# Kernel optimization log

Hardware: AMD Instinct MI355X
Metric: run time of the kernel (lower is better)

The kernel has to match this reference:

```python
import jax, jax.numpy as jnp
import numpy as np

K = 5  # kernel_size hardcoded in Net
PAD = (K - 1) // 2


def _patches(x):
    # x: [B, C, H, W] -> [B, C, K*K, H, W] (zero-padded sliding windows, like nn.Unfold)
    B, C, H, W = x.shape
    xp = jnp.pad(x, ((0, 0), (0, 0), (PAD, PAD), (PAD, PAD)))
    return jnp.stack([xp[:, :, i:i + H, j:j + W]
                      for i in range(K) for j in range(K)], axis=2)


def setup_inputs() -> dict:
    key = jax.random.key(0)
    k1, k2, k3 = jax.random.split(key, 3)
    x = jax.random.uniform(k1, (16, 1, 512, 512), dtype=jnp.float32)
    noise_var = jax.random.uniform(k2, (1,), dtype=jnp.float32)
    noise_bias = jax.random.uniform(k3, (1,), dtype=jnp.float32)
    return {"x": x, "noise_var": noise_var, "noise_bias": noise_bias}


def reference(x, noise_var, noise_bias):
    p = _patches(x)                          # [B, C, 25, H, W]
    s_var = jnp.var(p, axis=2, ddof=1)       # torch.var is unbiased by default
    mid = jnp.median(p, axis=2)              # odd window -> exact middle element
    y = x - noise_var / (s_var + 1e-10) * (x - mid + noise_bias)
    return jax.nn.relu(y)
```

## Files before the change

### kernel.cpp

```cpp
#include <hip/hip_runtime.h>

#define PAD 2
#define PX 4
#define BDX 16
#define BDY 16
#define TSX (BDX * PX)
#define TSY BDY
#define LTW (TSX + 2 * PAD)
#define LTH (TSY + 2 * PAD)
#define NCHUNK (LTH * LTW / 4)

typedef float float4u __attribute__((vector_size(16), aligned(4)));
typedef float v4f __attribute__((ext_vector_type(4)));

__device__ __forceinline__ float min3f(float a, float b, float c) {
    float r; asm("v_min3_f32 %0, %1, %2, %3" : "=v"(r) : "v"(a), "v"(b), "v"(c)); return r;
}
__device__ __forceinline__ float max3f(float a, float b, float c) {
    float r; asm("v_max3_f32 %0, %1, %2, %3" : "=v"(r) : "v"(a), "v"(b), "v"(c)); return r;
}
__device__ __forceinline__ float med3f(float a, float b, float c) {
    float r; asm("v_med3_f32 %0, %1, %2, %3" : "=v"(r) : "v"(a), "v"(b), "v"(c)); return r;
}

#define CE(a, b) { float _lo = fminf(a, b), _hi = fmaxf(a, b); (a) = _lo; (b) = _hi; }

#define MED9(q0, q1, q2, q3, q4, q5, q6, q7, q8) \
    CE(q1, q2) CE(q4, q5) CE(q7, q8) \
    CE(q0, q1) CE(q3, q4) CE(q6, q7) \
    CE(q1, q2) CE(q4, q5) CE(q7, q8) \
    CE(q0, q3) CE(q5, q8) CE(q4, q7) \
    CE(q3, q6) CE(q1, q4) CE(q2, q5) \
    CE(q4, q7) CE(q4, q2) CE(q6, q4) \
    CE(q4, q2)

__global__ __launch_bounds__(256) void denoise_median5_kernel(
    const float* __restrict__ x,
    const float* __restrict__ noise_var_p,
    const float* __restrict__ noise_bias_p,
    float* __restrict__ out,
    int H, int W)
{
    __shared__ float tile[LTH][LTW];

    const float noise_var  = noise_var_p[0];
    const float noise_bias = noise_bias_p[0];

    const int b      = blockIdx.z;
    const int tile_y = blockIdx.y * TSY;
    const int tile_x = blockIdx.x * TSX;
    const int tx = threadIdx.x;
    const int ty = threadIdx.y;
    const int tid = ty * BDX + tx;

    const float* __restrict__ img = x + (size_t)b * H * W;

    const bool interior = (blockIdx.x > 0) && (blockIdx.x < gridDim.x - 1) &&
                          (blockIdx.y > 0) && (blockIdx.y < gridDim.y - 1);
    if (interior) {
        const float* gbase = img + (size_t)(tile_y - PAD) * W + (tile_x - PAD);
        {
            const int i = tid;
            const int row = i / 17;
            const int cc  = i - row * 17;
            float4u v = *(const float4u*)(gbase + (size_t)row * W + cc * 4);
            *(float4u*)&tile[row][cc * 4] = v;
        }
        if (tid < NCHUNK - 256) {
            const int i = tid + 256;
            const int row = i / 17;
            const int cc  = i - row * 17;
            float4u v = *(const float4u*)(gbase + (size_t)row * W + cc * 4);
            *(float4u*)&tile[row][cc * 4] = v;
        }
    } else {
        for (int i = tid; i < LTH * LTW; i += BDX * BDY) {
            const int ly = i / LTW;
            const int lx = i - ly * LTW;
            const int gy = tile_y + ly - PAD;
            const int gx = tile_x + lx - PAD;
            float v = 0.0f;
            if (gy >= 0 && gy < H && gx >= 0 && gx < W)
                v = img[(size_t)gy * W + gx];
            tile[ly][lx] = v;
        }
    }
    __syncthreads();

    v4f A[5], D[5];
    #pragma unroll
    for (int r = 0; r < 5; ++r) {
        A[r] = *(const v4f*)&tile[ty + r][tx * PX];
        D[r] = *(const v4f*)&tile[ty + r][tx * PX + 4];
    }

    v4f SA = ((A[0] + A[1]) + (A[2] + A[3])) + A[4];
    v4f SD = ((D[0] + D[1]) + (D[2] + D[3])) + D[4];
    v4f QA = A[0] * A[0];
    v4f QD = D[0] * D[0];
    #pragma unroll
    for (int r = 1; r < 5; ++r) { QA = A[r] * A[r] + QA; QD = D[r] * D[r] + QD; }

    const float s8[8] = {SA.x, SA.y, SA.z, SA.w, SD.x, SD.y, SD.z, SD.w};
    const float q8[8] = {QA.x, QA.y, QA.z, QA.w, QD.x, QD.y, QD.z, QD.w};

    float sum5[PX], sq5[PX];
    sum5[0] = ((s8[0] + s8[1]) + (s8[2] + s8[3])) + s8[4];
    sq5[0]  = ((q8[0] + q8[1]) + (q8[2] + q8[3])) + q8[4];
    #pragma unroll
    for (int p = 1; p < PX; ++p) {
        sum5[p] = sum5[p - 1] - s8[p - 1] + s8[p + 4];
        sq5[p]  = sq5[p - 1]  - q8[p - 1] + q8[p + 4];
    }

    const float center[PX] = {A[2].z, A[2].w, D[2].x, D[2].y};

    float c[8][5];
    #pragma unroll
    for (int r = 0; r < 5; ++r) {
        c[0][r] = A[r].x; c[1][r] = A[r].y; c[2][r] = A[r].z; c[3][r] = A[r].w;
        c[4][r] = D[r].x; c[5][r] = D[r].y; c[6][r] = D[r].z; c[7][r] = D[r].w;
    }
    #pragma unroll
    for (int k = 0; k < 8; ++k) {
        const float a1 = fminf(c[k][0], c[k][1]), a2 = fmaxf(c[k][0], c[k][1]);
        const float b1 = fminf(c[k][2], c[k][3]), b2 = fmaxf(c[k][2], c[k][3]);
        const float cc = c[k][4];
        const float t1 = fminf(a2, b2), t3 = fmaxf(a1, b1);
        const float M  = fmaxf(a2, b2), m  = fminf(a1, b1);
        c[k][0] = fminf(m, cc);
        c[k][4] = fmaxf(M, cc);
        c[k][2] = med3f(t1, t3, cc);
        c[k][3] = max3f(t1, fminf(cc, M), t3);
        c[k][1] = min3f(t3, fmaxf(cc, m), t1);
    }

    float4 res;
    float* resp = (float*)&res;

    #pragma unroll
    for (int p = 0; p < PX; ++p) {
        float A1, A2, B1, B2, B3, C1, C2, C3, D1, D2, D3, E1, E2;
        {
            const float a1 = fminf(c[p][0], c[p+1][0]), a2 = fmaxf(c[p][0], c[p+1][0]);
            const float b1 = fminf(c[p+2][0], c[p+3][0]), b2 = fmaxf(c[p+2][0], c[p+3][0]);
            const float cc = c[p+4][0];
            const float M = fmaxf(a2, b2), t1 = fminf(a2, b2), t3 = fmaxf(a1, b1);
            A2 = fmaxf(M, cc);
            A1 = max3f(t1, fminf(cc, M), t3);
        }
        {
            const float a1 = fminf(c[p][1], c[p+1][1]), a2 = fmaxf(c[p][1], c[p+1][1]);
            const float b1 = fminf(c[p+2][1], c[p+3][1]), b2 = fmaxf(c[p+2][1], c[p+3][1]);
            const float cc = c[p+4][1];
            const float M = fmaxf(a2, b2), t1 = fminf(a2, b2), t3 = fmaxf(a1, b1);
            B3 = fmaxf(M, cc);
            B2 = max3f(t1, fminf(cc, M), t3);
            B1 = med3f(t1, t3, cc);
        }
        {
            const float a1 = fminf(c[p][2], c[p+1][2]), a2 = fmaxf(c[p][2], c[p+1][2]);
            const float b1 = fminf(c[p+2][2], c[p+3][2]), b2 = fmaxf(c[p+2][2], c[p+3][2]);
            const float cc = c[p+4][2];
            const float M = fmaxf(a2, b2), m = fminf(a1, b1);
            const float t1 = fminf(a2, b2), t3 = fmaxf(a1, b1);
            C2 = med3f(t1, t3, cc);
            C3 = max3f(t1, fminf(cc, M), t3);
            C1 = min3f(t3, fmaxf(cc, m), t1);
        }
        {
            const float a1 = fminf(c[p][3], c[p+1][3]), a2 = fmaxf(c[p][3], c[p+1][3]);
            const float b1 = fminf(c[p+2][3], c[p+3][3]), b2 = fmaxf(c[p+2][3], c[p+3][3]);
            const float cc = c[p+4][3];
            const float m = fminf(a1, b1), t1 = fminf(a2, b2), t3 = fmaxf(a1, b1);
            D1 = fminf(m, cc);
            D2 = min3f(t3, fmaxf(cc, m), t1);
            D3 = med3f(t1, t3, cc);
        }
        {
            const float a1 = fminf(c[p][4], c[p+1][4]), a2 = fmaxf(c[p][4], c[p+1][4]);
            const float b1 = fminf(c[p+2][4], c[p+3][4]), b2 = fmaxf(c[p+2][4], c[p+3][4]);
            const float cc = c[p+4][4];
            const float m = fminf(a1, b1), t1 = fminf(a2, b2), t3 = fmaxf(a1, b1);
            E1 = fminf(m, cc);
            E2 = min3f(t3, fmaxf(cc, m), t1);
        }

        const float mn1 = fminf(B3, D3);
        const float mn2 = fminf(C3, E2);
        const float mx1 = fmaxf(B1, D1);
        const float mx2 = fmaxf(A1, C1);

        float q0 = mx2, q1 = A2, q2 = B2, q3 = C2, q4 = D2,
              q5 = E1, q6 = mx1, q7 = mn1, q8 = mn2;
        MED9(q0, q1, q2, q3, q4, q5, q6, q7, q8);
        const float mid = q4;

        const float sum = sum5[p];
        const float sq  = sq5[p];
        const float mean = sum * (1.0f / 25.0f);
        float var = (sq - sum * mean) * (1.0f / 24.0f);
        var = fmaxf(var, 0.0f);

        const float xc = center[p];
        const float rr = __builtin_amdgcn_rcpf(var + 1e-10f);
        float y = xc - noise_var * rr * (xc - mid + noise_bias);
        resp[p] = fmaxf(y, 0.0f);
    }

    const int gy = tile_y + ty;
    const int gx = tile_x + tx * PX;
    *(float4*)&out[((size_t)b * H + gy) * W + gx] = res;
}

extern "C" void kernel_launch(void* const* d_in, const int* in_sizes, int n_in,
                              void* d_out, int out_size, void* d_ws, size_t ws_size,
                              hipStream_t stream)
{
    const float* x  = (const float*)d_in[0];
    const float* nv = (const float*)d_in[1];
    const float* nb = (const float*)d_in[2];
    float* out = (float*)d_out;

    const int H = 512, W = 512;
    const int B = in_sizes[0] / (H * W);

    dim3 block(BDX, BDY, 1);
    dim3 grid(W / TSX, H / TSY, B);
    denoise_median5_kernel<<<grid, block, 0, stream>>>(x, nv, nb, out, H, W);
}
```

Before: 31.65 us.

## Compute two output rows per thread, sharing sorted middle column rows

Each thread now produces a 4x2 output block. The four shared rows of each column are sorted once with a 4-element network, and the fifth row is inserted separately for the top and bottom windows. The row sums and sums of squares are shared between the two windows the same way. This is meant to cut the per-output sorting work and halve the number of blocks and LDS tile overlaps. The inline-asm min3/max3/med3 helpers are replaced with plain fminf/fmaxf, which depends on the compiler fusing them back into the 3-operand instructions. Register pressure rises.

```diff
diff --git a/kernel.cpp b/kernel.cpp
--- a/kernel.cpp
+++ b/kernel.cpp
@@ -2,10 +2,11 @@
 
 #define PAD 2
 #define PX 4
+#define PY 2
 #define BDX 16
 #define BDY 16
 #define TSX (BDX * PX)
-#define TSY BDY
+#define TSY (BDY * PY)
 #define LTW (TSX + 2 * PAD)
 #define LTH (TSY + 2 * PAD)
 #define NCHUNK (LTH * LTW / 4)
@@ -14,16 +15,25 @@
 typedef float v4f __attribute__((ext_vector_type(4)));
 
 __device__ __forceinline__ float min3f(float a, float b, float c) {
-    float r; asm("v_min3_f32 %0, %1, %2, %3" : "=v"(r) : "v"(a), "v"(b), "v"(c)); return r;
+    return fminf(fminf(a, b), c);
 }
 __device__ __forceinline__ float max3f(float a, float b, float c) {
-    float r; asm("v_max3_f32 %0, %1, %2, %3" : "=v"(r) : "v"(a), "v"(b), "v"(c)); return r;
+    return fmaxf(fmaxf(a, b), c);
 }
 __device__ __forceinline__ float med3f(float a, float b, float c) {
-    float r; asm("v_med3_f32 %0, %1, %2, %3" : "=v"(r) : "v"(a), "v"(b), "v"(c)); return r;
+    return fmaxf(fminf(a, b), fminf(fmaxf(a, b), c));
 }
 
 #define CE(a, b) { float _lo = fminf(a, b), _hi = fmaxf(a, b); (a) = _lo; (b) = _hi; }
+
+#define INSERT5(o0, o1, o2, o3, o4, s1, s2, s3, s4, e) { \
+    float _t  = fminf(s4, e);   o4 = fmaxf(s4, e); \
+    float _t2 = fminf(s3, _t);  o3 = fmaxf(s3, _t); \
+    float _t3 = fminf(s2, _t2); o2 = fmaxf(s2, _t2); \
+    o0 = fminf(s1, _t3);        o1 = fmaxf(s1, _t3); }
+
+#define SORT4(t0, t1, t2, t3) \
+    CE(t0, t1) CE(t2, t3) CE(t0, t2) CE(t1, t3) CE(t1, t2)
 
 #define MED9(q0, q1, q2, q3, q4, q5, q6, q7, q8) \
     CE(q1, q2) CE(q4, q5) CE(q7, q8) \
@@ -61,17 +71,18 @@
         const float* gbase = img + (size_t)(tile_y - PAD) * W + (tile_x - PAD);
         {
             const int i = tid;
-            const int row = i / 17;
-            const int cc  = i - row * 17;
-            float4u v = *(const float4u*)(gbase + (size_t)row * W + cc * 4);
-            *(float4u*)&tile[row][cc * 4] = v;
-        }
-        if (tid < NCHUNK - 256) {
+            const int row = i / 17, cc = i - row * 17;
+            *(float4u*)&tile[row][cc * 4] = *(const float4u*)(gbase + (size_t)row * W + cc * 4);
+        }
+        {
             const int i = tid + 256;
-            const int row = i / 17;
-            const int cc  = i - row * 17;
-            float4u v = *(const float4u*)(gbase + (size_t)row * W + cc * 4);
-            *(float4u*)&tile[row][cc * 4] = v;
+            const int row = i / 17, cc = i - row * 17;
+            *(float4u*)&tile[row][cc * 4] = *(const float4u*)(gbase + (size_t)row * W + cc * 4);
+        }
+        if (tid < NCHUNK - 512) {
+            const int i = tid + 512;
+            const int row = i / 17, cc = i - row * 17;
+            *(float4u*)&tile[row][cc * 4] = *(const float4u*)(gbase + (size_t)row * W + cc * 4);
         }
     } else {
         for (int i = tid; i < LTH * LTW; i += BDX * BDY) {
@@ -87,130 +98,159 @@
     }
     __syncthreads();
 
-    v4f A[5], D[5];
+    v4f A[6], Dq[6];
     #pragma unroll
-    for (int r = 0; r < 5; ++r) {
-        A[r] = *(const v4f*)&tile[ty + r][tx * PX];
-        D[r] = *(const v4f*)&tile[ty + r][tx * PX + 4];
-    }
-
-    v4f SA = ((A[0] + A[1]) + (A[2] + A[3])) + A[4];
-    v4f SD = ((D[0] + D[1]) + (D[2] + D[3])) + D[4];
-    v4f QA = A[0] * A[0];
-    v4f QD = D[0] * D[0];
+    for (int r = 0; r < 6; ++r) {
+        A[r]  = *(const v4f*)&tile[ty * PY + r][tx * PX];
+        Dq[r] = *(const v4f*)&tile[ty * PY + r][tx * PX + 4];
+    }
+
+    v4f SAsh = (A[1] + A[2]) + (A[3] + A[4]);
+    v4f SDsh = (Dq[1] + Dq[2]) + (Dq[3] + Dq[4]);
+    v4f QAsh = A[1] * A[1];  QAsh = A[2] * A[2] + QAsh;
+    QAsh = A[3] * A[3] + QAsh;  QAsh = A[4] * A[4] + QAsh;
+    v4f QDsh = Dq[1] * Dq[1];  QDsh = Dq[2] * Dq[2] + QDsh;
+    QDsh = Dq[3] * Dq[3] + QDsh;  QDsh = Dq[4] * Dq[4] + QDsh;
+
+    const v4f SA_A = SAsh + A[0],  SD_A = SDsh + Dq[0];
+    const v4f SA_B = SAsh + A[5],  SD_B = SDsh + Dq[5];
+    const v4f QA_A = A[0] * A[0] + QAsh,   QD_A = Dq[0] * Dq[0] + QDsh;
+    const v4f QA_B = A[5] * A[5] + QAsh,   QD_B = Dq[5] * Dq[5] + QDsh;
+
+    float sum5A[PX], sq5A[PX], sum5B[PX], sq5B[PX];
+    {
+        const float sA8[8] = {SA_A.x, SA_A.y, SA_A.z, SA_A.w, SD_A.x, SD_A.y, SD_A.z, SD_A.w};
+        const float qA8[8] = {QA_A.x, QA_A.y, QA_A.z, QA_A.w, QD_A.x, QD_A.y, QD_A.z, QD_A.w};
+        const float sB8[8] = {SA_B.x, SA_B.y, SA_B.z, SA_B.w, SD_B.x, SD_B.y, SD_B.z, SD_B.w};
+        const float qB8[8] = {QA_B.x, QA_B.y, QA_B.z, QA_B.w, QD_B.x, QD_B.y, QD_B.z, QD_B.w};
+        sum5A[0] = ((sA8[0] + sA8[1]) + (sA8[2] + sA8[3])) + sA8[4];
+        sq5A[0]  = ((qA8[0] + qA8[1]) + (qA8[2] + qA8[3])) + qA8[4];
+        sum5B[0] = ((sB8[0] + sB8[1]) + (sB8[2] + sB8[3])) + sB8[4];
+        sq5B[0]  = ((qB8[0] + qB8[1]) + (qB8[2] + qB8[3])) + qB8[4];
+        #pragma unroll
+        for (int p = 1; p < PX; ++p) {
+            sum5A[p] = sum5A[p - 1] - sA8[p - 1] + sA8[p + 4];
+            sq5A[p]  = sq5A[p - 1]  - qA8[p - 1] + qA8[p + 4];
+            sum5B[p] = sum5B[p - 1] - sB8[p - 1] + sB8[p + 4];
+            sq5B[p]  = sq5B[p - 1]  - qB8[p - 1] + qB8[p + 4];
+        }
+    }
+
+    const float centerA[PX] = {A[2].z, A[2].w, Dq[2].x, Dq[2].y};
+    const float centerB[PX] = {A[3].z, A[3].w, Dq[3].x, Dq[3].y};
+
+    float c[8][6];
     #pragma unroll
-    for (int r = 1; r < 5; ++r) { QA = A[r] * A[r] + QA; QD = D[r] * D[r] + QD; }
-
-    const float s8[8] = {SA.x, SA.y, SA.z, SA.w, SD.x, SD.y, SD.z, SD.w};
-    const float q8[8] = {QA.x, QA.y, QA.z, QA.w, QD.x, QD.y, QD.z, QD.w};
-
-    float sum5[PX], sq5[PX];
-    sum5[0] = ((s8[0] + s8[1]) + (s8[2] + s8[3])) + s8[4];
-    sq5[0]  = ((q8[0] + q8[1]) + (q8[2] + q8[3])) + q8[4];
-    #pragma unroll
-    for (int p = 1; p < PX; ++p) {
-        sum5[p] = sum5[p - 1] - s8[p - 1] + s8[p + 4];
-        sq5[p]  = sq5[p - 1]  - q8[p - 1] + q8[p + 4];
-    }
-
-    const float center[PX] = {A[2].z, A[2].w, D[2].x, D[2].y};
-
-    float c[8][5];
-    #pragma unroll
-    for (int r = 0; r < 5; ++r) {
-        c[0][r] = A[r].x; c[1][r] = A[r].y; c[2][r] = A[r].z; c[3][r] = A[r].w;
-        c[4][r] = D[r].x; c[5][r] = D[r].y; c[6][r] = D[r].z; c[7][r] = D[r].w;
+    for (int r = 0; r < 6; ++r) {
+        c[0][r] = A[r].x;  c[1][r] = A[r].y;  c[2][r] = A[r].z;  c[3][r] = A[r].w;
+        c[4][r] = Dq[r].x; c[5][r] = Dq[r].y; c[6][r] = Dq[r].z; c[7][r] = Dq[r].w;
     }
     #pragma unroll
     for (int k = 0; k < 8; ++k) {
-        const float a1 = fminf(c[k][0], c[k][1]), a2 = fmaxf(c[k][0], c[k][1]);
-        const float b1 = fminf(c[k][2], c[k][3]), b2 = fmaxf(c[k][2], c[k][3]);
-        const float cc = c[k][4];
-        const float t1 = fminf(a2, b2), t3 = fmaxf(a1, b1);
-        const float M  = fmaxf(a2, b2), m  = fminf(a1, b1);
-        c[k][0] = fminf(m, cc);
-        c[k][4] = fmaxf(M, cc);
-        c[k][2] = med3f(t1, t3, cc);
-        c[k][3] = max3f(t1, fminf(cc, M), t3);
-        c[k][1] = min3f(t3, fmaxf(cc, m), t1);
-    }
-
-    float4 res;
-    float* resp = (float*)&res;
-
-    #pragma unroll
-    for (int p = 0; p < PX; ++p) {
-        float A1, A2, B1, B2, B3, C1, C2, C3, D1, D2, D3, E1, E2;
-        {
-            const float a1 = fminf(c[p][0], c[p+1][0]), a2 = fmaxf(c[p][0], c[p+1][0]);
-            const float b1 = fminf(c[p+2][0], c[p+3][0]), b2 = fmaxf(c[p+2][0], c[p+3][0]);
-            const float cc = c[p+4][0];
-            const float M = fmaxf(a2, b2), t1 = fminf(a2, b2), t3 = fmaxf(a1, b1);
-            A2 = fmaxf(M, cc);
-            A1 = max3f(t1, fminf(cc, M), t3);
-        }
-        {
-            const float a1 = fminf(c[p][1], c[p+1][1]), a2 = fmaxf(c[p][1], c[p+1][1]);
-            const float b1 = fminf(c[p+2][1], c[p+3][1]), b2 = fmaxf(c[p+2][1], c[p+3][1]);
-            const float cc = c[p+4][1];
-            const float M = fmaxf(a2, b2), t1 = fminf(a2, b2), t3 = fmaxf(a1, b1);
-            B3 = fmaxf(M, cc);
-            B2 = max3f(t1, fminf(cc, M), t3);
-            B1 = med3f(t1, t3, cc);
-        }
-        {
-            const float a1 = fminf(c[p][2], c[p+1][2]), a2 = fmaxf(c[p][2], c[p+1][2]);
-            const float b1 = fminf(c[p+2][2], c[p+3][2]), b2 = fmaxf(c[p+2][2], c[p+3][2]);
-            const float cc = c[p+4][2];
-            const float M = fmaxf(a2, b2), m = fminf(a1, b1);
-            const float t1 = fminf(a2, b2), t3 = fmaxf(a1, b1);
-            C2 = med3f(t1, t3, cc);
-            C3 = max3f(t1, fminf(cc, M), t3);
-            C1 = min3f(t3, fmaxf(cc, m), t1);
-        }
-        {
-            const float a1 = fminf(c[p][3], c[p+1][3]), a2 = fmaxf(c[p][3], c[p+1][3]);
-            const float b1 = fminf(c[p+2][3], c[p+3][3]), b2 = fmaxf(c[p+2][3], c[p+3][3]);
-            const float cc = c[p+4][3];
-            const float m = fminf(a1, b1), t1 = fminf(a2, b2), t3 = fmaxf(a1, b1);
-            D1 = fminf(m, cc);
-            D2 = min3f(t3, fmaxf(cc, m), t1);
-            D3 = med3f(t1, t3, cc);
-        }
-        {
-            const float a1 = fminf(c[p][4], c[p+1][4]), a2 = fmaxf(c[p][4], c[p+1][4]);
-            const float b1 = fminf(c[p+2][4], c[p+3][4]), b2 = fmaxf(c[p+2][4], c[p+3][4]);
-            const float cc = c[p+4][4];
-            const float m = fminf(a1, b1), t1 = fminf(a2, b2), t3 = fmaxf(a1, b1);
-            E1 = fminf(m, cc);
-            E2 = min3f(t3, fmaxf(cc, m), t1);
-        }
-
-        const float mn1 = fminf(B3, D3);
-        const float mn2 = fminf(C3, E2);
-        const float mx1 = fmaxf(B1, D1);
-        const float mx2 = fmaxf(A1, C1);
-
-        float q0 = mx2, q1 = A2, q2 = B2, q3 = C2, q4 = D2,
-              q5 = E1, q6 = mx1, q7 = mn1, q8 = mn2;
-        MED9(q0, q1, q2, q3, q4, q5, q6, q7, q8);
-        const float mid = q4;
-
-        const float sum = sum5[p];
-        const float sq  = sq5[p];
-        const float mean = sum * (1.0f / 25.0f);
-        float var = (sq - sum * mean) * (1.0f / 24.0f);
-        var = fmaxf(var, 0.0f);
-
-        const float xc = center[p];
-        const float rr = __builtin_amdgcn_rcpf(var + 1e-10f);
-        float y = xc - noise_var * rr * (xc - mid + noise_bias);
-        resp[p] = fmaxf(y, 0.0f);
-    }
-
-    const int gy = tile_y + ty;
-    const int gx = tile_x + tx * PX;
-    *(float4*)&out[((size_t)b * H + gy) * W + gx] = res;
+        SORT4(c[k][1], c[k][2], c[k][3], c[k][4]);
+    }
+
+    float* outp = out + (size_t)b * H * W;
+    const int oy0 = tile_y + ty * PY;
+    const int ox  = tile_x + tx * PX;
+
+    auto run_window = [&](const float (&col)[8][5], const float (&center)[PX],
+                          const float (&sum5)[PX], const float (&sq5)[PX]) -> float4 {
+        float4 res;
+        float* resp = (float*)&res;
+        #pragma unroll
+        for (int p = 0; p < PX; ++p) {
+            float A1, A2, B1, B2, B3, C1, C2, C3, D1, D2, D3, E1, E2;
+            {
+                const float a1 = fminf(col[p][0], col[p+1][0]), a2 = fmaxf(col[p][0], col[p+1][0]);
+                const float b1 = fminf(col[p+2][0], col[p+3][0]), b2 = fmaxf(col[p+2][0], col[p+3][0]);
+                const float cc = col[p+4][0];
+                const float M = fmaxf(a2, b2), t1 = fminf(a2, b2), t3 = fmaxf(a1, b1);
+                A2 = fmaxf(M, cc);
+                A1 = max3f(t1, fminf(cc, M), t3);
+            }
+            {
+                const float a1 = fminf(col[p][1], col[p+1][1]), a2 = fmaxf(col[p][1], col[p+1][1]);
+                const float b1 = fminf(col[p+2][1], col[p+3][1]), b2 = fmaxf(col[p+2][1], col[p+3][1]);
+                const float cc = col[p+4][1];
+                const float M = fmaxf(a2, b2), t1 = fminf(a2, b2), t3 = fmaxf(a1, b1);
+                B3 = fmaxf(M, cc);
+                B2 = max3f(t1, fminf(cc, M), t3);
+                B1 = med3f(t1, t3, cc);
+            }
+            {
+                const float a1 = fminf(col[p][2], col[p+1][2]), a2 = fmaxf(col[p][2], col[p+1][2]);
+                const float b1 = fminf(col[p+2][2], col[p+3][2]), b2 = fmaxf(col[p+2][2], col[p+3][2]);
+                const float cc = col[p+4][2];
+                const float M = fmaxf(a2, b2), m = fminf(a1, b1);
+                const float t1 = fminf(a2, b2), t3 = fmaxf(a1, b1);
+                C2 = med3f(t1, t3, cc);
+                C3 = max3f(t1, fminf(cc, M), t3);
+                C1 = min3f(t3, fmaxf(cc, m), t1);
+            }
+            {
+                const float a1 = fminf(col[p][3], col[p+1][3]), a2 = fmaxf(col[p][3], col[p+1][3]);
+                const float b1 = fminf(col[p+2][3], col[p+3][3]), b2 = fmaxf(col[p+2][3], col[p+3][3]);
+                const float cc = col[p+4][3];
+                const float m = fminf(a1, b1), t1 = fminf(a2, b2), t3 = fmaxf(a1, b1);
+                D1 = fminf(m, cc);
+                D2 = min3f(t3, fmaxf(cc, m), t1);
+                D3 = med3f(t1, t3, cc);
+            }
+            {
+                const float a1 = fminf(col[p][4], col[p+1][4]), a2 = fmaxf(col[p][4], col[p+1][4]);
+                const float b1 = fminf(col[p+2][4], col[p+3][4]), b2 = fmaxf(col[p+2][4], col[p+3][4]);
+                const float cc = col[p+4][4];
+                const float m = fminf(a1, b1), t1 = fminf(a2, b2), t3 = fmaxf(a1, b1);
+                E1 = fminf(m, cc);
+                E2 = min3f(t3, fmaxf(cc, m), t1);
+            }
+
+            const float mn1 = fminf(B3, D3);
+            const float mn2 = fminf(C3, E2);
+            const float mx1 = fmaxf(B1, D1);
+            const float mx2 = fmaxf(A1, C1);
+
+            float q0 = mx2, q1 = A2, q2 = B2, q3 = C2, q4 = D2,
+                  q5 = E1, q6 = mx1, q7 = mn1, q8 = mn2;
+            MED9(q0, q1, q2, q3, q4, q5, q6, q7, q8);
+            const float mid = q4;
+
+            const float sum = sum5[p];
+            const float sq  = sq5[p];
+            const float mean = sum * (1.0f / 25.0f);
+            float var = (sq - sum * mean) * (1.0f / 24.0f);
+            var = fmaxf(var, 0.0f);
+
+            const float xc = center[p];
+            const float rr = __builtin_amdgcn_rcpf(var + 1e-10f);
+            float y = xc - noise_var * rr * (xc - mid + noise_bias);
+            resp[p] = fmaxf(y, 0.0f);
+        }
+        return res;
+    };
+
+    {
+        float colA[8][5];
+        #pragma unroll
+        for (int k = 0; k < 8; ++k) {
+            INSERT5(colA[k][0], colA[k][1], colA[k][2], colA[k][3], colA[k][4],
+                    c[k][1], c[k][2], c[k][3], c[k][4], c[k][0]);
+        }
+        float4 resA = run_window(colA, centerA, sum5A, sq5A);
+        *(float4*)&outp[(size_t)oy0 * W + ox] = resA;
+    }
+
+    {
+        float colB[8][5];
+        #pragma unroll
+        for (int k = 0; k < 8; ++k) {
+            INSERT5(colB[k][0], colB[k][1], colB[k][2], colB[k][3], colB[k][4],
+                    c[k][1], c[k][2], c[k][3], c[k][4], c[k][5]);
+        }
+        float4 resB = run_window(colB, centerB, sum5B, sq5B);
+        *(float4*)&outp[(size_t)(oy0 + 1) * W + ox] = resB;
+    }
 }
 
 extern "C" void kernel_launch(void* const* d_in, const int* in_sizes, int n_in,
```

New measurement: 31.71 us. Within noise of the previous version (+0.2%).

## Split block into per-wave LDS slices loaded via global_load_lds without block barrier

Applied to the files above, without the earlier changes.

Each of the four waves now loads its own 8x68 halo slice straight into LDS with global_load_lds and waits only on its own counters, so the block-wide __syncthreads is gone. Each wave handles 4 output rows instead of the block sharing one 20-row tile. This lets waves run independently and skips the VGPR round trip on loads, but it reloads more halo rows per block (8 rows per 4 rows of output instead of 20 per 16). The inline-asm min3/max3/med3 are also replaced with plain fminf/fmaxf expressions, left for the compiler to fuse back.

```diff
diff --git a/kernel.cpp b/kernel.cpp
--- a/kernel.cpp
+++ b/kernel.cpp
@@ -2,25 +2,28 @@
 
 #define PAD 2
 #define PX 4
-#define BDX 16
-#define BDY 16
-#define TSX (BDX * PX)
-#define TSY BDY
-#define LTW (TSX + 2 * PAD)
-#define LTH (TSY + 2 * PAD)
-#define NCHUNK (LTH * LTW / 4)
-
-typedef float float4u __attribute__((vector_size(16), aligned(4)));
+#define WROWS 4
+#define NWAVES 4
+#define TSX 64
+#define TSY (WROWS * NWAVES)
+#define LTW 68
+#define LTH (WROWS + 2 * PAD)
+#define SLICE (LTH * LTW)
+#define NCHUNK (SLICE / 4)
+
 typedef float v4f __attribute__((ext_vector_type(4)));
 
+typedef __attribute__((address_space(1))) const void ga_void;
+typedef __attribute__((address_space(3))) void ls_void;
+
 __device__ __forceinline__ float min3f(float a, float b, float c) {
-    float r; asm("v_min3_f32 %0, %1, %2, %3" : "=v"(r) : "v"(a), "v"(b), "v"(c)); return r;
+    return fminf(fminf(a, b), c);
 }
 __device__ __forceinline__ float max3f(float a, float b, float c) {
-    float r; asm("v_max3_f32 %0, %1, %2, %3" : "=v"(r) : "v"(a), "v"(b), "v"(c)); return r;
+    return fmaxf(fmaxf(a, b), c);
 }
 __device__ __forceinline__ float med3f(float a, float b, float c) {
-    float r; asm("v_med3_f32 %0, %1, %2, %3" : "=v"(r) : "v"(a), "v"(b), "v"(c)); return r;
+    return fmaxf(fminf(a, b), fminf(fmaxf(a, b), c));
 }
 
 #define CE(a, b) { float _lo = fminf(a, b), _hi = fmaxf(a, b); (a) = _lo; (b) = _hi; }
@@ -41,65 +44,81 @@
     float* __restrict__ out,
     int H, int W)
 {
-    __shared__ float tile[LTH][LTW];
+    __shared__ float lds[NWAVES * SLICE];
 
     const float noise_var  = noise_var_p[0];
     const float noise_bias = noise_bias_p[0];
 
+    const int tid  = threadIdx.x;
+    const int lane = tid & 63;
+    const int wid  = tid >> 6;
+
     const int b      = blockIdx.z;
-    const int tile_y = blockIdx.y * TSY;
     const int tile_x = blockIdx.x * TSX;
-    const int tx = threadIdx.x;
-    const int ty = threadIdx.y;
-    const int tid = ty * BDX + tx;
+    const int wy     = blockIdx.y * TSY + wid * WROWS;
+    const int gy0    = wy - PAD;
+    const int gx0    = tile_x - PAD;
 
     const float* __restrict__ img = x + (size_t)b * H * W;
-
-    const bool interior = (blockIdx.x > 0) && (blockIdx.x < gridDim.x - 1) &&
-                          (blockIdx.y > 0) && (blockIdx.y < gridDim.y - 1);
+    float* __restrict__ ldsbase = &lds[wid * SLICE];
+
+    const bool interior = (blockIdx.x >= 1) && (blockIdx.x <= gridDim.x - 2) &&
+                          (wy >= PAD) && (wy <= H - LTH + PAD);
+
     if (interior) {
-        const float* gbase = img + (size_t)(tile_y - PAD) * W + (tile_x - PAD);
-        {
-            const int i = tid;
-            const int row = i / 17;
-            const int cc  = i - row * 17;
-            float4u v = *(const float4u*)(gbase + (size_t)row * W + cc * 4);
-            *(float4u*)&tile[row][cc * 4] = v;
-        }
-        if (tid < NCHUNK - 256) {
-            const int i = tid + 256;
-            const int row = i / 17;
-            const int cc  = i - row * 17;
-            float4u v = *(const float4u*)(gbase + (size_t)row * W + cc * 4);
-            *(float4u*)&tile[row][cc * 4] = v;
-        }
+        const float* gbase = img + (size_t)gy0 * W + gx0;
+        #pragma unroll
+        for (int batch = 0; batch < 2; ++batch) {
+            const int chunk = batch * 64 + lane;
+            const int row = chunk / 17;
+            const int cc  = chunk - row * 17;
+            const float* gsrc = gbase + (size_t)row * W + cc * 4;
+            __builtin_amdgcn_global_load_lds((ga_void*)gsrc,
+                                             (ls_void*)(ldsbase + batch * 256),
+                                             16, 0, 0);
+        }
+        if (lane < NCHUNK - 128) {
+            const int chunk = 128 + lane;
+            const int row = chunk / 17;
+            const int cc  = chunk - row * 17;
+            const float* gsrc = gbase + (size_t)row * W + cc * 4;
+            __builtin_amdgcn_global_load_lds((ga_void*)gsrc,
+                                             (ls_void*)(ldsbase + 512),
+                                             16, 0, 0);
+        }
+        asm volatile("s_waitcnt vmcnt(0)" ::: "memory");
+        __builtin_amdgcn_sched_barrier(0);
     } else {
-        for (int i = tid; i < LTH * LTW; i += BDX * BDY) {
+        for (int i = lane; i < SLICE; i += 64) {
             const int ly = i / LTW;
             const int lx = i - ly * LTW;
-            const int gy = tile_y + ly - PAD;
-            const int gx = tile_x + lx - PAD;
+            const int gy = gy0 + ly;
+            const int gx = gx0 + lx;
             float v = 0.0f;
-            if (gy >= 0 && gy < H && gx >= 0 && gx < W)
+            if ((unsigned)gy < (unsigned)H && (unsigned)gx < (unsigned)W)
                 v = img[(size_t)gy * W + gx];
-            tile[ly][lx] = v;
-        }
-    }
-    __syncthreads();
-
-    v4f A[5], D[5];
+            ldsbase[i] = v;
+        }
+        asm volatile("s_waitcnt lgkmcnt(0)" ::: "memory");
+        __builtin_amdgcn_sched_barrier(0);
+    }
+
+    const int lx16 = lane & 15;
+    const int lrow = lane >> 4;
+
+    v4f A[5], Dq[5];
     #pragma unroll
     for (int r = 0; r < 5; ++r) {
-        A[r] = *(const v4f*)&tile[ty + r][tx * PX];
-        D[r] = *(const v4f*)&tile[ty + r][tx * PX + 4];
+        A[r]  = *(const v4f*)&ldsbase[(lrow + r) * LTW + lx16 * 4];
+        Dq[r] = *(const v4f*)&ldsbase[(lrow + r) * LTW + lx16 * 4 + 4];
     }
 
     v4f SA = ((A[0] + A[1]) + (A[2] + A[3])) + A[4];
-    v4f SD = ((D[0] + D[1]) + (D[2] + D[3])) + D[4];
+    v4f SD = ((Dq[0] + Dq[1]) + (Dq[2] + Dq[3])) + Dq[4];
     v4f QA = A[0] * A[0];
-    v4f QD = D[0] * D[0];
-    #pragma unroll
-    for (int r = 1; r < 5; ++r) { QA = A[r] * A[r] + QA; QD = D[r] * D[r] + QD; }
+    v4f QD = Dq[0] * Dq[0];
+    #pragma unroll
+    for (int r = 1; r < 5; ++r) { QA = A[r] * A[r] + QA; QD = Dq[r] * Dq[r] + QD; }
 
     const float s8[8] = {SA.x, SA.y, SA.z, SA.w, SD.x, SD.y, SD.z, SD.w};
     const float q8[8] = {QA.x, QA.y, QA.z, QA.w, QD.x, QD.y, QD.z, QD.w};
@@ -113,13 +132,13 @@
         sq5[p]  = sq5[p - 1]  - q8[p - 1] + q8[p + 4];
     }
 
-    const float center[PX] = {A[2].z, A[2].w, D[2].x, D[2].y};
+    const float center[PX] = {A[2].z, A[2].w, Dq[2].x, Dq[2].y};
 
     float c[8][5];
     #pragma unroll
     for (int r = 0; r < 5; ++r) {
-        c[0][r] = A[r].x; c[1][r] = A[r].y; c[2][r] = A[r].z; c[3][r] = A[r].w;
-        c[4][r] = D[r].x; c[5][r] = D[r].y; c[6][r] = D[r].z; c[7][r] = D[r].w;
+        c[0][r] = A[r].x;  c[1][r] = A[r].y;  c[2][r] = A[r].z;  c[3][r] = A[r].w;
+        c[4][r] = Dq[r].x; c[5][r] = Dq[r].y; c[6][r] = Dq[r].z; c[7][r] = Dq[r].w;
     }
     #pragma unroll
     for (int k = 0; k < 8; ++k) {
@@ -208,9 +227,9 @@
         resp[p] = fmaxf(y, 0.0f);
     }
 
-    const int gy = tile_y + ty;
-    const int gx = tile_x + tx * PX;
-    *(float4*)&out[((size_t)b * H + gy) * W + gx] = res;
+    const int orow = wy + lrow;
+    const int ox   = tile_x + lx16 * PX;
+    *(float4*)&out[((size_t)b * H + orow) * W + ox] = res;
 }
 
 extern "C" void kernel_launch(void* const* d_in, const int* in_sizes, int n_in,
@@ -225,7 +244,7 @@
     const int H = 512, W = 512;
     const int B = in_sizes[0] / (H * W);
 
-    dim3 block(BDX, BDY, 1);
+    dim3 block(256, 1, 1);
     dim3 grid(W / TSX, H / TSY, B);
     denoise_median5_kernel<<<grid, block, 0, stream>>>(x, nv, nb, out, H, W);
 }
```

Result: slower. 32.47 us (+2.6%).

## Halve pixels per thread to two and compute stats from sorted columns

Applied to the files above, without the earlier changes.

Each thread now computes 2 output pixels instead of 4, which doubles the grid size and shrinks the shared tile to 36 columns, loaded with a single float4 pass. Column sums and sums of squares are now taken from the sorted column values, which is valid because sums are order-invariant. The inline-asm min3/max3/med3 are replaced by plain fminf/fmaxf expressions that the compiler may or may not fuse back. The change trades more threads and less register pressure for more redundant halo loads and sorting work per output pixel.

```diff
diff --git a/kernel.cpp b/kernel.cpp
--- a/kernel.cpp
+++ b/kernel.cpp
@@ -1,26 +1,26 @@
 #include <hip/hip_runtime.h>
 
 #define PAD 2
-#define PX 4
+#define PXT 2
 #define BDX 16
 #define BDY 16
-#define TSX (BDX * PX)
+#define TSX (BDX * PXT)
 #define TSY BDY
 #define LTW (TSX + 2 * PAD)
 #define LTH (TSY + 2 * PAD)
 #define NCHUNK (LTH * LTW / 4)
 
 typedef float float4u __attribute__((vector_size(16), aligned(4)));
-typedef float v4f __attribute__((ext_vector_type(4)));
+typedef float v2f __attribute__((ext_vector_type(2)));
 
 __device__ __forceinline__ float min3f(float a, float b, float c) {
-    float r; asm("v_min3_f32 %0, %1, %2, %3" : "=v"(r) : "v"(a), "v"(b), "v"(c)); return r;
+    return fminf(fminf(a, b), c);
 }
 __device__ __forceinline__ float max3f(float a, float b, float c) {
-    float r; asm("v_max3_f32 %0, %1, %2, %3" : "=v"(r) : "v"(a), "v"(b), "v"(c)); return r;
+    return fmaxf(fmaxf(a, b), c);
 }
 __device__ __forceinline__ float med3f(float a, float b, float c) {
-    float r; asm("v_med3_f32 %0, %1, %2, %3" : "=v"(r) : "v"(a), "v"(b), "v"(c)); return r;
+    return fmaxf(fminf(a, b), fminf(fmaxf(a, b), c));
 }
 
 #define CE(a, b) { float _lo = fminf(a, b), _hi = fmaxf(a, b); (a) = _lo; (b) = _hi; }
@@ -58,20 +58,11 @@
     const bool interior = (blockIdx.x > 0) && (blockIdx.x < gridDim.x - 1) &&
                           (blockIdx.y > 0) && (blockIdx.y < gridDim.y - 1);
     if (interior) {
-        const float* gbase = img + (size_t)(tile_y - PAD) * W + (tile_x - PAD);
-        {
-            const int i = tid;
-            const int row = i / 17;
-            const int cc  = i - row * 17;
-            float4u v = *(const float4u*)(gbase + (size_t)row * W + cc * 4);
-            *(float4u*)&tile[row][cc * 4] = v;
-        }
-        if (tid < NCHUNK - 256) {
-            const int i = tid + 256;
-            const int row = i / 17;
-            const int cc  = i - row * 17;
-            float4u v = *(const float4u*)(gbase + (size_t)row * W + cc * 4);
-            *(float4u*)&tile[row][cc * 4] = v;
+        if (tid < NCHUNK) {
+            const int row = tid / 9;
+            const int cc  = tid - row * 9;
+            const float* gsrc = img + (size_t)(tile_y - PAD + row) * W + (tile_x - PAD) + cc * 4;
+            *(float4u*)&tile[row][cc * 4] = *(const float4u*)gsrc;
         }
     } else {
         for (int i = tid; i < LTH * LTW; i += BDX * BDY) {
@@ -80,49 +71,29 @@
             const int gy = tile_y + ly - PAD;
             const int gx = tile_x + lx - PAD;
             float v = 0.0f;
-            if (gy >= 0 && gy < H && gx >= 0 && gx < W)
+            if ((unsigned)gy < (unsigned)H && (unsigned)gx < (unsigned)W)
                 v = img[(size_t)gy * W + gx];
             tile[ly][lx] = v;
         }
     }
     __syncthreads();
 
-    v4f A[5], D[5];
+    float c[6][5];
     #pragma unroll
     for (int r = 0; r < 5; ++r) {
-        A[r] = *(const v4f*)&tile[ty + r][tx * PX];
-        D[r] = *(const v4f*)&tile[ty + r][tx * PX + 4];
-    }
-
-    v4f SA = ((A[0] + A[1]) + (A[2] + A[3])) + A[4];
-    v4f SD = ((D[0] + D[1]) + (D[2] + D[3])) + D[4];
-    v4f QA = A[0] * A[0];
-    v4f QD = D[0] * D[0];
-    #pragma unroll
-    for (int r = 1; r < 5; ++r) { QA = A[r] * A[r] + QA; QD = D[r] * D[r] + QD; }
-
-    const float s8[8] = {SA.x, SA.y, SA.z, SA.w, SD.x, SD.y, SD.z, SD.w};
-    const float q8[8] = {QA.x, QA.y, QA.z, QA.w, QD.x, QD.y, QD.z, QD.w};
-
-    float sum5[PX], sq5[PX];
-    sum5[0] = ((s8[0] + s8[1]) + (s8[2] + s8[3])) + s8[4];
-    sq5[0]  = ((q8[0] + q8[1]) + (q8[2] + q8[3])) + q8[4];
-    #pragma unroll
-    for (int p = 1; p < PX; ++p) {
-        sum5[p] = sum5[p - 1] - s8[p - 1] + s8[p + 4];
-        sq5[p]  = sq5[p - 1]  - q8[p - 1] + q8[p + 4];
-    }
-
-    const float center[PX] = {A[2].z, A[2].w, D[2].x, D[2].y};
-
-    float c[8][5];
-    #pragma unroll
-    for (int r = 0; r < 5; ++r) {
-        c[0][r] = A[r].x; c[1][r] = A[r].y; c[2][r] = A[r].z; c[3][r] = A[r].w;
-        c[4][r] = D[r].x; c[5][r] = D[r].y; c[6][r] = D[r].z; c[7][r] = D[r].w;
-    }
-    #pragma unroll
-    for (int k = 0; k < 8; ++k) {
+        const v2f a = *(const v2f*)&tile[ty + r][tx * PXT + 0];
+        const v2f d = *(const v2f*)&tile[ty + r][tx * PXT + 2];
+        const v2f e = *(const v2f*)&tile[ty + r][tx * PXT + 4];
+        c[0][r] = a.x; c[1][r] = a.y;
+        c[2][r] = d.x; c[3][r] = d.y;
+        c[4][r] = e.x; c[5][r] = e.y;
+    }
+
+    const float center0 = c[2][2];
+    const float center1 = c[3][2];
+
+    #pragma unroll
+    for (int k = 0; k < 6; ++k) {
         const float a1 = fminf(c[k][0], c[k][1]), a2 = fmaxf(c[k][0], c[k][1]);
         const float b1 = fminf(c[k][2], c[k][3]), b2 = fmaxf(c[k][2], c[k][3]);
         const float cc = c[k][4];
@@ -135,11 +106,25 @@
         c[k][1] = min3f(t3, fmaxf(cc, m), t1);
     }
 
-    float4 res;
-    float* resp = (float*)&res;
-
-    #pragma unroll
-    for (int p = 0; p < PX; ++p) {
+    float sc[6], qc[6];
+    #pragma unroll
+    for (int k = 0; k < 6; ++k) {
+        sc[k] = ((c[k][0] + c[k][1]) + (c[k][2] + c[k][3])) + c[k][4];
+        float qq = c[k][0] * c[k][0];
+        qq = fmaf(c[k][1], c[k][1], qq);
+        qq = fmaf(c[k][2], c[k][2], qq);
+        qq = fmaf(c[k][3], c[k][3], qq);
+        qc[k] = fmaf(c[k][4], c[k][4], qq);
+    }
+    const float sum0 = ((sc[0] + sc[1]) + (sc[2] + sc[3])) + sc[4];
+    const float sq0  = ((qc[0] + qc[1]) + (qc[2] + qc[3])) + qc[4];
+    const float sum1 = sum0 - sc[0] + sc[5];
+    const float sq1  = sq0  - qc[0] + qc[5];
+
+    v2f res;
+
+    #pragma unroll
+    for (int p = 0; p < PXT; ++p) {
         float A1, A2, B1, B2, B3, C1, C2, C3, D1, D2, D3, E1, E2;
         {
             const float a1 = fminf(c[p][0], c[p+1][0]), a2 = fmaxf(c[p][0], c[p+1][0]);
@@ -196,21 +181,21 @@
         MED9(q0, q1, q2, q3, q4, q5, q6, q7, q8);
         const float mid = q4;
 
-        const float sum = sum5[p];
-        const float sq  = sq5[p];
+        const float sum = (p == 0) ? sum0 : sum1;
+        const float sq  = (p == 0) ? sq0  : sq1;
         const float mean = sum * (1.0f / 25.0f);
         float var = (sq - sum * mean) * (1.0f / 24.0f);
         var = fmaxf(var, 0.0f);
 
-        const float xc = center[p];
+        const float xc = (p == 0) ? center0 : center1;
         const float rr = __builtin_amdgcn_rcpf(var + 1e-10f);
         float y = xc - noise_var * rr * (xc - mid + noise_bias);
-        resp[p] = fmaxf(y, 0.0f);
+        res[p] = fmaxf(y, 0.0f);
     }
 
     const int gy = tile_y + ty;
-    const int gx = tile_x + tx * PX;
-    *(float4*)&out[((size_t)b * H + gy) * W + gx] = res;
+    const int gx = tile_x + tx * PXT;
+    *(v2f*)&out[((size_t)b * H + gy) * W + gx] = res;
 }
 
 extern "C" void kernel_launch(void* const* d_in, const int* in_sizes, int n_in,
```

Measured after the change: 34.04 us. 7.6% more time.
